# Kernel optimization log

Measured on AMD Instinct MI355X. Metric: run time of the kernel, lower is better.

## Reference

```python
import jax, jax.numpy as jnp
import numpy as np

N = 100000
E = 3200000
IN_C = 256
HID = 32
OUT_C = 64


def setup_inputs() -> dict:
    key = jax.random.key(0)
    k = jax.random.split(key, 7)
    x = jax.random.normal(k[0], (N, IN_C), dtype=jnp.float32)
    edge_index = jax.random.randint(k[1], (2, E), 0, N, dtype=jnp.int64)
    # Glorot-style init for GCNConv weights, zero bias (PyG default)
    w1 = jax.random.normal(k[2], (IN_C, HID), dtype=jnp.float32) / np.sqrt(IN_C)
    b1 = jnp.zeros((HID,), dtype=jnp.float32)
    w2 = jax.random.normal(k[3], (HID, OUT_C), dtype=jnp.float32) / np.sqrt(HID)
    b2 = jnp.zeros((OUT_C,), dtype=jnp.float32)
    return {"x": x, "edge_index": edge_index, "w1": w1, "b1": b1, "w2": w2, "b2": b2}


def _gcn_conv(x, src, dst, norm, w, b):
    # linear transform then normalized scatter-add aggregation (flow: src -> dst)
    h = x @ w                                   # [N, F_out]
    msg = h[src] * norm[:, None]                # [E, F_out] gather + scale
    out = jax.ops.segment_sum(msg, dst, num_segments=N)
    return out + b


def reference(x, edge_index, w1, b1, w2, b2):
    src = edge_index[0]
    dst = edge_index[1]
    # symmetric GCN normalization, no self loops (add_self_loops=False)
    deg = jax.ops.segment_sum(jnp.ones((E,), dtype=x.dtype), dst, num_segments=N)
    dinv = jnp.where(deg > 0, jax.lax.rsqrt(jnp.maximum(deg, 1e-12)), 0.0)
    norm = dinv[src] * dinv[dst]                # [E]
    h = jax.nn.relu(_gcn_conv(x, src, dst, norm, w1, b1))
    # dropout: identity in eval mode
    h = _gcn_conv(h, src, dst, norm, w2, b2)
    return jax.nn.log_softmax(h, axis=1)
```

## Files before the change

kernel.cpp:

```cpp
#include <hip/hip_runtime.h>


constexpr int NN   = 100000;
constexpr int EE   = 3200000;
constexpr int INC  = 256;
constexpr int HIDC = 32;
constexpr int OUTC = 64;

__global__ __launch_bounds__(256) void deg_kernel(const int* __restrict__ dst,
                                                  unsigned* __restrict__ deg, int E) {
    int i = blockIdx.x * 256 + threadIdx.x;
    if (i < E) atomicAdd(&deg[dst[i]], 1u);
}

__global__ __launch_bounds__(256) void dinv_kernel(const unsigned* __restrict__ deg,
                                                   float* __restrict__ dinv, int n) {
    int i = blockIdx.x * 256 + threadIdx.x;
    if (i < n) {
        unsigned d = deg[i];
        dinv[i] = d ? rsqrtf((float)d) : 0.f;
    }
}

__global__ __launch_bounds__(256) void scan1_kernel(const unsigned* __restrict__ deg,
                                                    int* __restrict__ rowptr,
                                                    unsigned* __restrict__ aux, int n) {
    __shared__ unsigned s[256];
    int t = threadIdx.x;
    int i = blockIdx.x * 256 + t;
    unsigned v = (i < n) ? deg[i] : 0u;
    s[t] = v;
    __syncthreads();
#pragma unroll
    for (int off = 1; off < 256; off <<= 1) {
        unsigned u = (t >= off) ? s[t - off] : 0u;
        __syncthreads();
        s[t] += u;
        __syncthreads();
    }
    if (i < n) rowptr[i + 1] = (int)s[t];
    if (t == 255) aux[blockIdx.x] = s[255];
}

__global__ __launch_bounds__(512) void scan2_kernel(unsigned* __restrict__ aux, int nb) {
    __shared__ unsigned s[512];
    int t = threadIdx.x;
    unsigned v = (t < nb) ? aux[t] : 0u;
    s[t] = v;
    __syncthreads();
#pragma unroll
    for (int off = 1; off < 512; off <<= 1) {
        unsigned u = (t >= off) ? s[t - off] : 0u;
        __syncthreads();
        s[t] += u;
        __syncthreads();
    }
    if (t < nb) aux[t] = s[t] - v;
}

__global__ __launch_bounds__(256) void scan3_kernel(int* __restrict__ rowptr,
                                                    const unsigned* __restrict__ aux, int n) {
    int i = blockIdx.x * 256 + threadIdx.x;
    if (i < n) rowptr[i + 1] += (int)aux[blockIdx.x];
    if (i == 0) rowptr[0] = 0;
}

__global__ __launch_bounds__(256) void scatter_kernel(const int* __restrict__ src,
                                                      const int* __restrict__ dst,
                                                      const int* __restrict__ rowptr,
                                                      unsigned* __restrict__ fill,
                                                      int* __restrict__ srcS, int E) {
    int e = blockIdx.x * 256 + threadIdx.x;
    if (e >= E) return;
    int d = dst[e];
    int pos = rowptr[d] + (int)atomicAdd(&fill[d], 1u);
    srcS[pos] = src[e];
}

__global__ __launch_bounds__(256) void gemm1_kernel(const float* __restrict__ x,
                                                    const float* __restrict__ w1,
                                                    float* __restrict__ h1) {
    __shared__ float ws[INC * HIDC];
    __shared__ float xs[8][INC];
    int t = threadIdx.x;
    for (int i = t; i < INC * HIDC; i += 256) ws[i] = w1[i];
    int row0 = blockIdx.x * 8;
    const float4* x4 = reinterpret_cast<const float4*>(x + (size_t)row0 * INC);
    float4* xs4 = reinterpret_cast<float4*>(&xs[0][0]);
    xs4[t]       = x4[t];
    xs4[t + 256] = x4[t + 256];
    __syncthreads();
    int g = t >> 5;
    int col = t & 31;
    float acc = 0.f;
#pragma unroll 8
    for (int k = 0; k < INC; ++k)
        acc = fmaf(xs[g][k], ws[k * HIDC + col], acc);
    h1[(size_t)(row0 + g) * HIDC + col] = acc;
}

__global__ __launch_bounds__(256) void agg1_kernel(const int* __restrict__ rowptr,
                                                   const int* __restrict__ srcS,
                                                   const float* __restrict__ dinv,
                                                   const float* __restrict__ h1,
                                                   const float* __restrict__ b1,
                                                   float* __restrict__ h1a, int n) {
    int t = threadIdx.x;
    int grp = t >> 5, f = t & 31;
    int row = blockIdx.x * 8 + grp;
    if (row >= n) return;
    int e = rowptr[row], end = rowptr[row + 1];
    float acc = 0.f;
    for (; e + 4 <= end; e += 4) {
        int s0 = srcS[e], s1 = srcS[e + 1], s2 = srcS[e + 2], s3 = srcS[e + 3];
        float d0 = dinv[s0], d1 = dinv[s1], d2 = dinv[s2], d3 = dinv[s3];
        acc = fmaf(h1[(size_t)s0 * HIDC + f], d0, acc);
        acc = fmaf(h1[(size_t)s1 * HIDC + f], d1, acc);
        acc = fmaf(h1[(size_t)s2 * HIDC + f], d2, acc);
        acc = fmaf(h1[(size_t)s3 * HIDC + f], d3, acc);
    }
    for (; e < end; ++e) {
        int s = srcS[e];
        acc = fmaf(h1[(size_t)s * HIDC + f], dinv[s], acc);
    }
    float v = acc * dinv[row] + b1[f];
    h1a[(size_t)row * HIDC + f] = v > 0.f ? v : 0.f;
}

__global__ __launch_bounds__(256) void gemm2_kernel(const float* __restrict__ h,
                                                    const float* __restrict__ w2,
                                                    float* __restrict__ g) {
    __shared__ float ws[HIDC * OUTC];
    __shared__ float xs[4][HIDC];
    int t = threadIdx.x;
    for (int i = t; i < HIDC * OUTC; i += 256) ws[i] = w2[i];
    int wv = t >> 6, lane = t & 63;
    int row = blockIdx.x * 4 + wv;
    if (lane < HIDC) xs[wv][lane] = h[(size_t)row * HIDC + lane];
    __syncthreads();
    float acc = 0.f;
#pragma unroll
    for (int k = 0; k < HIDC; ++k)
        acc = fmaf(xs[wv][k], ws[k * OUTC + lane], acc);
    g[(size_t)row * OUTC + lane] = acc;
}

__global__ __launch_bounds__(256) void agg2_lsm_kernel(const int* __restrict__ rowptr,
                                                       const int* __restrict__ srcS,
                                                       const float* __restrict__ dinv,
                                                       const float* __restrict__ g,
                                                       const float* __restrict__ b2,
                                                       float* __restrict__ out, int n) {
    int t = threadIdx.x;
    int wv = t >> 6, lane = t & 63;
    int row = blockIdx.x * 4 + wv;
    if (row >= n) return;
    int e = rowptr[row], end = rowptr[row + 1];
    float acc = 0.f;
    for (; e + 4 <= end; e += 4) {
        int s0 = srcS[e], s1 = srcS[e + 1], s2 = srcS[e + 2], s3 = srcS[e + 3];
        float d0 = dinv[s0], d1 = dinv[s1], d2 = dinv[s2], d3 = dinv[s3];
        acc = fmaf(g[(size_t)s0 * OUTC + lane], d0, acc);
        acc = fmaf(g[(size_t)s1 * OUTC + lane], d1, acc);
        acc = fmaf(g[(size_t)s2 * OUTC + lane], d2, acc);
        acc = fmaf(g[(size_t)s3 * OUTC + lane], d3, acc);
    }
    for (; e < end; ++e) {
        int s = srcS[e];
        acc = fmaf(g[(size_t)s * OUTC + lane], dinv[s], acc);
    }
    float v = acc * dinv[row] + b2[lane];
    float m = v;
#pragma unroll
    for (int off = 32; off; off >>= 1)
        m = fmaxf(m, __shfl_xor(m, off));
    float sm = expf(v - m);
#pragma unroll
    for (int off = 32; off; off >>= 1)
        sm += __shfl_xor(sm, off);
    out[(size_t)row * OUTC + lane] = v - m - logf(sm);
}

extern "C" void kernel_launch(void* const* d_in, const int* in_sizes, int n_in,
                              void* d_out, int out_size, void* d_ws, size_t ws_size,
                              hipStream_t stream) {
    const float* x  = (const float*)d_in[0];
    const int*   ei = (const int*)d_in[1];
    const float* w1 = (const float*)d_in[2];
    const float* b1 = (const float*)d_in[3];
    const float* w2 = (const float*)d_in[4];
    const float* b2 = (const float*)d_in[5];
    float* out = (float*)d_out;

    const int n = NN, E = EE;
    const int* src = ei;
    const int* dst = ei + E;

    unsigned* deg  = (unsigned*)d_ws;
    unsigned* fill = deg + n;
    float* dinv    = (float*)(fill + n);
    int* rowptr    = (int*)(dinv + n);
    unsigned* aux  = (unsigned*)(rowptr + n + 1);
    int* srcS      = (int*)(aux + 1024);
    float* h1      = (float*)(srcS + E);
    float* h1a     = h1 + (size_t)n * HIDC;
    float* g       = h1a + (size_t)n * HIDC;

    const int nbE = (E + 255) / 256;
    const int nbN = (n + 255) / 256;

    hipMemsetAsync(deg, 0, sizeof(unsigned) * (size_t)2 * n, stream);

    deg_kernel<<<nbE, 256, 0, stream>>>(dst, deg, E);
    dinv_kernel<<<nbN, 256, 0, stream>>>(deg, dinv, n);
    scan1_kernel<<<nbN, 256, 0, stream>>>(deg, rowptr, aux, n);
    scan2_kernel<<<1, 512, 0, stream>>>(aux, nbN);
    scan3_kernel<<<nbN, 256, 0, stream>>>(rowptr, aux, n);
    scatter_kernel<<<nbE, 256, 0, stream>>>(src, dst, rowptr, fill, srcS, E);

    gemm1_kernel<<<n / 8, 256, 0, stream>>>(x, w1, h1);
    agg1_kernel<<<n / 8, 256, 0, stream>>>(rowptr, srcS, dinv, h1, b1, h1a, n);
    gemm2_kernel<<<n / 4, 256, 0, stream>>>(h1a, w2, g);
    agg2_lsm_kernel<<<n / 4, 256, 0, stream>>>(rowptr, srcS, dinv, g, b2, out, n);
}
```

Before: 783.6 us.

## Aggregate before second linear layer and pack source dinv into CSR entries

Reorders the second GCN layer to aggregate the 32-wide hidden features first and then apply W2, fused with bias and log-softmax. This halves the gathered bytes per edge in the second aggregation compared with gathering 64-wide rows. The CSR array now stores (src, dinv[src]) pairs, which removes the dependent dinv gather in both aggregations at the cost of doubling index storage. The gather loops are also unrolled to 8 edges to keep more loads in flight.

```diff
diff --git a/kernel.cpp b/kernel.cpp
--- a/kernel.cpp
+++ b/kernel.cpp
@@ -68,13 +68,15 @@
 __global__ __launch_bounds__(256) void scatter_kernel(const int* __restrict__ src,
                                                       const int* __restrict__ dst,
                                                       const int* __restrict__ rowptr,
+                                                      const float* __restrict__ dinv,
                                                       unsigned* __restrict__ fill,
-                                                      int* __restrict__ srcS, int E) {
+                                                      int2* __restrict__ srcS, int E) {
     int e = blockIdx.x * 256 + threadIdx.x;
     if (e >= E) return;
     int d = dst[e];
+    int s = src[e];
     int pos = rowptr[d] + (int)atomicAdd(&fill[d], 1u);
-    srcS[pos] = src[e];
+    srcS[pos] = make_int2(s, __float_as_int(dinv[s]));
 }
 
 __global__ __launch_bounds__(256) void gemm1_kernel(const float* __restrict__ x,
@@ -100,7 +102,7 @@
 }
 
 __global__ __launch_bounds__(256) void agg1_kernel(const int* __restrict__ rowptr,
-                                                   const int* __restrict__ srcS,
+                                                   const int2* __restrict__ srcS,
                                                    const float* __restrict__ dinv,
                                                    const float* __restrict__ h1,
                                                    const float* __restrict__ b1,
@@ -111,65 +113,83 @@
     if (row >= n) return;
     int e = rowptr[row], end = rowptr[row + 1];
     float acc = 0.f;
-    for (; e + 4 <= end; e += 4) {
-        int s0 = srcS[e], s1 = srcS[e + 1], s2 = srcS[e + 2], s3 = srcS[e + 3];
-        float d0 = dinv[s0], d1 = dinv[s1], d2 = dinv[s2], d3 = dinv[s3];
-        acc = fmaf(h1[(size_t)s0 * HIDC + f], d0, acc);
-        acc = fmaf(h1[(size_t)s1 * HIDC + f], d1, acc);
-        acc = fmaf(h1[(size_t)s2 * HIDC + f], d2, acc);
-        acc = fmaf(h1[(size_t)s3 * HIDC + f], d3, acc);
+    for (; e + 8 <= end; e += 8) {
+        int2 p0 = srcS[e],     p1 = srcS[e + 1], p2 = srcS[e + 2], p3 = srcS[e + 3];
+        int2 p4 = srcS[e + 4], p5 = srcS[e + 5], p6 = srcS[e + 6], p7 = srcS[e + 7];
+        float v0 = h1[(size_t)p0.x * HIDC + f], v1 = h1[(size_t)p1.x * HIDC + f];
+        float v2 = h1[(size_t)p2.x * HIDC + f], v3 = h1[(size_t)p3.x * HIDC + f];
+        float v4 = h1[(size_t)p4.x * HIDC + f], v5 = h1[(size_t)p5.x * HIDC + f];
+        float v6 = h1[(size_t)p6.x * HIDC + f], v7 = h1[(size_t)p7.x * HIDC + f];
+        acc = fmaf(v0, __int_as_float(p0.y), acc);
+        acc = fmaf(v1, __int_as_float(p1.y), acc);
+        acc = fmaf(v2, __int_as_float(p2.y), acc);
+        acc = fmaf(v3, __int_as_float(p3.y), acc);
+        acc = fmaf(v4, __int_as_float(p4.y), acc);
+        acc = fmaf(v5, __int_as_float(p5.y), acc);
+        acc = fmaf(v6, __int_as_float(p6.y), acc);
+        acc = fmaf(v7, __int_as_float(p7.y), acc);
     }
     for (; e < end; ++e) {
-        int s = srcS[e];
-        acc = fmaf(h1[(size_t)s * HIDC + f], dinv[s], acc);
+        int2 p = srcS[e];
+        acc = fmaf(h1[(size_t)p.x * HIDC + f], __int_as_float(p.y), acc);
     }
     float v = acc * dinv[row] + b1[f];
     h1a[(size_t)row * HIDC + f] = v > 0.f ? v : 0.f;
 }
 
-__global__ __launch_bounds__(256) void gemm2_kernel(const float* __restrict__ h,
-                                                    const float* __restrict__ w2,
-                                                    float* __restrict__ g) {
-    __shared__ float ws[HIDC * OUTC];
-    __shared__ float xs[4][HIDC];
-    int t = threadIdx.x;
-    for (int i = t; i < HIDC * OUTC; i += 256) ws[i] = w2[i];
-    int wv = t >> 6, lane = t & 63;
-    int row = blockIdx.x * 4 + wv;
-    if (lane < HIDC) xs[wv][lane] = h[(size_t)row * HIDC + lane];
-    __syncthreads();
-    float acc = 0.f;
-#pragma unroll
-    for (int k = 0; k < HIDC; ++k)
-        acc = fmaf(xs[wv][k], ws[k * OUTC + lane], acc);
-    g[(size_t)row * OUTC + lane] = acc;
-}
-
-__global__ __launch_bounds__(256) void agg2_lsm_kernel(const int* __restrict__ rowptr,
-                                                       const int* __restrict__ srcS,
-                                                       const float* __restrict__ dinv,
-                                                       const float* __restrict__ g,
-                                                       const float* __restrict__ b2,
-                                                       float* __restrict__ out, int n) {
-    int t = threadIdx.x;
-    int wv = t >> 6, lane = t & 63;
-    int row = blockIdx.x * 4 + wv;
+__global__ __launch_bounds__(256) void agg2_kernel(const int* __restrict__ rowptr,
+                                                   const int2* __restrict__ srcS,
+                                                   const float* __restrict__ dinv,
+                                                   const float* __restrict__ h1a,
+                                                   float* __restrict__ z2, int n) {
+    int t = threadIdx.x;
+    int grp = t >> 5, f = t & 31;
+    int row = blockIdx.x * 8 + grp;
     if (row >= n) return;
     int e = rowptr[row], end = rowptr[row + 1];
     float acc = 0.f;
-    for (; e + 4 <= end; e += 4) {
-        int s0 = srcS[e], s1 = srcS[e + 1], s2 = srcS[e + 2], s3 = srcS[e + 3];
-        float d0 = dinv[s0], d1 = dinv[s1], d2 = dinv[s2], d3 = dinv[s3];
-        acc = fmaf(g[(size_t)s0 * OUTC + lane], d0, acc);
-        acc = fmaf(g[(size_t)s1 * OUTC + lane], d1, acc);
-        acc = fmaf(g[(size_t)s2 * OUTC + lane], d2, acc);
-        acc = fmaf(g[(size_t)s3 * OUTC + lane], d3, acc);
+    for (; e + 8 <= end; e += 8) {
+        int2 p0 = srcS[e],     p1 = srcS[e + 1], p2 = srcS[e + 2], p3 = srcS[e + 3];
+        int2 p4 = srcS[e + 4], p5 = srcS[e + 5], p6 = srcS[e + 6], p7 = srcS[e + 7];
+        float v0 = h1a[(size_t)p0.x * HIDC + f], v1 = h1a[(size_t)p1.x * HIDC + f];
+        float v2 = h1a[(size_t)p2.x * HIDC + f], v3 = h1a[(size_t)p3.x * HIDC + f];
+        float v4 = h1a[(size_t)p4.x * HIDC + f], v5 = h1a[(size_t)p5.x * HIDC + f];
+        float v6 = h1a[(size_t)p6.x * HIDC + f], v7 = h1a[(size_t)p7.x * HIDC + f];
+        acc = fmaf(v0, __int_as_float(p0.y), acc);
+        acc = fmaf(v1, __int_as_float(p1.y), acc);
+        acc = fmaf(v2, __int_as_float(p2.y), acc);
+        acc = fmaf(v3, __int_as_float(p3.y), acc);
+        acc = fmaf(v4, __int_as_float(p4.y), acc);
+        acc = fmaf(v5, __int_as_float(p5.y), acc);
+        acc = fmaf(v6, __int_as_float(p6.y), acc);
+        acc = fmaf(v7, __int_as_float(p7.y), acc);
     }
     for (; e < end; ++e) {
-        int s = srcS[e];
-        acc = fmaf(g[(size_t)s * OUTC + lane], dinv[s], acc);
-    }
-    float v = acc * dinv[row] + b2[lane];
+        int2 p = srcS[e];
+        acc = fmaf(h1a[(size_t)p.x * HIDC + f], __int_as_float(p.y), acc);
+    }
+    z2[(size_t)row * HIDC + f] = acc * dinv[row];
+}
+
+__global__ __launch_bounds__(256) void gemmlsm_kernel(const float* __restrict__ z2,
+                                                      const float* __restrict__ w2,
+                                                      const float* __restrict__ b2,
+                                                      float* __restrict__ out, int n) {
+    __shared__ float ws[HIDC * OUTC];
+    __shared__ float zs[4][HIDC];
+    int t = threadIdx.x;
+    for (int i = t; i < HIDC * OUTC; i += 256) ws[i] = w2[i];
+    int row0 = blockIdx.x * 4;
+    if (t < 4 * HIDC) zs[t >> 5][t & 31] = z2[(size_t)row0 * HIDC + t];
+    __syncthreads();
+    int wv = t >> 6, lane = t & 63;
+    int row = row0 + wv;
+    if (row >= n) return;
+    float acc = 0.f;
+#pragma unroll
+    for (int k = 0; k < HIDC; ++k)
+        acc = fmaf(zs[wv][k], ws[k * OUTC + lane], acc);
+    float v = acc + b2[lane];
     float m = v;
 #pragma unroll
     for (int off = 32; off; off >>= 1)
@@ -201,10 +221,10 @@
     float* dinv    = (float*)(fill + n);
     int* rowptr    = (int*)(dinv + n);
     unsigned* aux  = (unsigned*)(rowptr + n + 1);
-    int* srcS      = (int*)(aux + 1024);
+    int2* srcS     = (int2*)(aux + 1024);
     float* h1      = (float*)(srcS + E);
     float* h1a     = h1 + (size_t)n * HIDC;
-    float* g       = h1a + (size_t)n * HIDC;
+    float* z2      = h1a + (size_t)n * HIDC;
 
     const int nbE = (E + 255) / 256;
     const int nbN = (n + 255) / 256;
@@ -216,10 +236,10 @@
     scan1_kernel<<<nbN, 256, 0, stream>>>(deg, rowptr, aux, n);
     scan2_kernel<<<1, 512, 0, stream>>>(aux, nbN);
     scan3_kernel<<<nbN, 256, 0, stream>>>(rowptr, aux, n);
-    scatter_kernel<<<nbE, 256, 0, stream>>>(src, dst, rowptr, fill, srcS, E);
+    scatter_kernel<<<nbE, 256, 0, stream>>>(src, dst, rowptr, dinv, fill, srcS, E);
 
     gemm1_kernel<<<n / 8, 256, 0, stream>>>(x, w1, h1);
     agg1_kernel<<<n / 8, 256, 0, stream>>>(rowptr, srcS, dinv, h1, b1, h1a, n);
-    gemm2_kernel<<<n / 4, 256, 0, stream>>>(h1a, w2, g);
-    agg2_lsm_kernel<<<n / 4, 256, 0, stream>>>(rowptr, srcS, dinv, g, b2, out, n);
-}
+    agg2_kernel<<<n / 8, 256, 0, stream>>>(rowptr, srcS, dinv, h1a, z2, n);
+    gemmlsm_kernel<<<n / 4, 256, 0, stream>>>(z2, w2, b2, out, n);
+}
```

Result: faster. 729.8 us (-6.9%).
